# Kernel optimization log

Hardware: AMD Instinct MI355X
Metric: run time of the kernel (lower is better)

The kernel has to match this reference:

```python
import jax, jax.numpy as jnp
import numpy as np

TOP_K = 2


def setup_inputs() -> dict:
    key = jax.random.key(0)
    ks = jax.random.split(key, 5)
    B, S, H, F, E = 1, 2048, 1024, 3584, 8
    scale_h = 1.0 / np.sqrt(H)
    scale_f = 1.0 / np.sqrt(F)
    return {
        "hidden_states": jax.random.normal(ks[0], (B, S, H), dtype=jnp.float32),
        "gate_w": jax.random.normal(ks[1], (E, H), dtype=jnp.float32) * scale_h,
        "w1": jax.random.normal(ks[2], (E, H, F), dtype=jnp.float32) * scale_h,
        "w3": jax.random.normal(ks[3], (E, H, F), dtype=jnp.float32) * scale_h,
        "w2": jax.random.normal(ks[4], (E, F, H), dtype=jnp.float32) * scale_f,
    }


def reference(hidden_states, gate_w, w1, w2, w3):
    B, S, H = hidden_states.shape
    E = gate_w.shape[0]
    x = hidden_states.reshape(-1, H)  # [T, H]
    # Router: logits -> fp32 softmax -> top-k -> renormalize
    router_logits = x @ gate_w.T  # [T, E]
    probs = jax.nn.softmax(router_logits.astype(jnp.float32), axis=-1)
    top_w, top_idx = jax.lax.top_k(probs, TOP_K)  # [T, K]
    top_w = top_w / jnp.sum(top_w, axis=-1, keepdims=True)
    top_w = top_w.astype(x.dtype)
    # Dense combine weights [T, E]: routing weight if expert selected else 0
    combine = jnp.sum(jax.nn.one_hot(top_idx, E, dtype=x.dtype) * top_w[..., None], axis=1)
    # Per-expert SwiGLU FFN, weighted-summed (loop over small fixed E)
    out = jnp.zeros_like(x)
    for e in range(E):
        h = jax.nn.silu(x @ w1[e]) * (x @ w3[e])  # [T, F]
        out = out + (h @ w2[e]) * combine[:, e:e + 1]
    return out.reshape(B, S, H), router_logits
```

## Files before the change

kernel.cpp:

```cpp
#include <hip/hip_runtime.h>
#include <cstdint>
#include <cstddef>

#define Tt 2048
#define Hh 1024
#define Ff 3584
#define Ee 8
#define ROWS_CAP 5120

#define OFF_CTRL   0u
#define OFF_TOKE   256u
#define OFF_TOKW   (256u + 16384u)
#define OFF_ROWMAP (256u + 32768u)
#define OFF_ROWW   (256u + 32768u + 20480u)
#define OFF_XG     (1ull << 20)
#define OFF_G      (12ull << 20)

typedef __attribute__((ext_vector_type(8))) short bf16x8;
typedef __attribute__((ext_vector_type(4))) float f32x4;

__device__ __forceinline__ unsigned short f2bf(float f) {
  unsigned int u = __float_as_uint(f);
  u += 0x7fffu + ((u >> 16) & 1u);
  return (unsigned short)(u >> 16);
}

__device__ __forceinline__ unsigned pkbf(float a, float b) {
  unsigned r;
  asm("v_cvt_pk_bf16_f32 %0, %1, %2" : "=v"(r) : "v"(a), "v"(b));
  return r;
}

__device__ __forceinline__ void gload_lds16(const void* g, void* l) {
  auto gp = (const __attribute__((address_space(1))) char*)(uintptr_t)g;
  auto lp = (__attribute__((address_space(3))) char*)(uintptr_t)l;
  __builtin_amdgcn_global_load_lds(gp, lp, 16, 0, 0);
}

__device__ __forceinline__ bf16x8 frg(const char* lds, int row, int gc) {
  return *(const bf16x8*)(lds + row * 64 + ((gc ^ ((row >> 1) & 3)) * 16));
}

__global__ __launch_bounds__(256) void router_kernel(
    const float* __restrict__ x, const float* __restrict__ gw,
    float* __restrict__ logits_out, int* __restrict__ tok_e,
    float* __restrict__ tok_w, int* __restrict__ ctrl) {
  const int lane = threadIdx.x & 63;
  const int t = blockIdx.x * 4 + (threadIdx.x >> 6);
  const float4* xp = (const float4*)(x + (size_t)t * Hh + lane * 16);
  float4 x0 = xp[0], x1 = xp[1], x2 = xp[2], x3 = xp[3];
  float lg[Ee];
#pragma unroll
  for (int e = 0; e < Ee; ++e) {
    const float4* gp = (const float4*)(gw + e * Hh + lane * 16);
    float4 g0 = gp[0], g1 = gp[1], g2 = gp[2], g3 = gp[3];
    float s = x0.x*g0.x + x0.y*g0.y + x0.z*g0.z + x0.w*g0.w
            + x1.x*g1.x + x1.y*g1.y + x1.z*g1.z + x1.w*g1.w
            + x2.x*g2.x + x2.y*g2.y + x2.z*g2.z + x2.w*g2.w
            + x3.x*g3.x + x3.y*g3.y + x3.z*g3.z + x3.w*g3.w;
#pragma unroll
    for (int o = 32; o; o >>= 1) s += __shfl_xor(s, o);
    lg[e] = s;
  }
  if (lane == 0) {
    float m = lg[0];
#pragma unroll
    for (int e = 1; e < Ee; ++e) m = fmaxf(m, lg[e]);
    float p[Ee];
#pragma unroll
    for (int e = 0; e < Ee; ++e) p[e] = expf(lg[e] - m);
    int a0 = 0;
#pragma unroll
    for (int e = 1; e < Ee; ++e) if (p[e] > p[a0]) a0 = e;
    int a1 = (a0 == 0) ? 1 : 0;
#pragma unroll
    for (int e = 0; e < Ee; ++e) if (e != a0 && p[e] > p[a1]) a1 = e;
    float rs = p[a0] + p[a1];
    float w0 = p[a0] / rs, w1 = p[a1] / rs;
#pragma unroll
    for (int e = 0; e < Ee; ++e) logits_out[(size_t)t * Ee + e] = lg[e];
    tok_e[t * 2] = a0; tok_e[t * 2 + 1] = a1;
    tok_w[t * 2] = w0; tok_w[t * 2 + 1] = w1;
    atomicAdd(&ctrl[a0], 1); atomicAdd(&ctrl[a1], 1);
  }
}

__global__ void offsets_kernel(int* ctrl) {
  if (threadIdx.x == 0) {
    int acc = 0;
    for (int e = 0; e < Ee; ++e) {
      ctrl[16 + e] = acc;
      acc += ((ctrl[e] + 127) >> 7) << 7;
    }
    ctrl[16 + Ee] = acc;
  }
}

__global__ __launch_bounds__(512) void assign_kernel(
    int* ctrl, const int* __restrict__ tok_e, const float* __restrict__ tok_w,
    int* __restrict__ rowmap, float* __restrict__ roww) {
  int i = blockIdx.x * 512 + threadIdx.x;
  if (i < 2 * Tt) {
    int e = tok_e[i];
    int pos = atomicAdd(&ctrl[8 + e], 1);
    int r = ctrl[16 + e] + pos;
    rowmap[r] = i >> 1;
    roww[r] = tok_w[i];
  }
  if (i < Ee * 128) {
    int e = i >> 7, pd = i & 127;
    int o = ctrl[16 + e], o1 = ctrl[16 + e + 1], c = ctrl[e];
    int r = o + c + pd;
    if (r < o1) { rowmap[r] = -1; roww[r] = 0.f; }
  }
}

__global__ __launch_bounds__(128) void gather_kernel(
    const float* __restrict__ x, const int* __restrict__ ctrl,
    const int* __restrict__ rowmap, unsigned short* __restrict__ Xg) {
  int r = blockIdx.x;
  if (r >= ctrl[16 + Ee]) return;
  int t = rowmap[r];
  int j = threadIdx.x;
  uint4 v = make_uint4(0u, 0u, 0u, 0u);
  if (t >= 0) {
    const float4* xp = (const float4*)(x + (size_t)t * Hh + j * 8);
    float4 a = xp[0], b = xp[1];
    v.x = (unsigned)f2bf(a.x) | ((unsigned)f2bf(a.y) << 16);
    v.y = (unsigned)f2bf(a.z) | ((unsigned)f2bf(a.w) << 16);
    v.z = (unsigned)f2bf(b.x) | ((unsigned)f2bf(b.y) << 16);
    v.w = (unsigned)f2bf(b.z) | ((unsigned)f2bf(b.w) << 16);
  }
  *(uint4*)(Xg + (size_t)r * Hh + j * 8) = v;
}

__global__ __launch_bounds__(512, 4) void ffn13_fused(
    const unsigned short* __restrict__ Xg, const float* __restrict__ w1,
    const float* __restrict__ w3, const int* __restrict__ ctrl,
    unsigned short* __restrict__ G) {
  __shared__ alignas(16) char sA[2][8192], sB1[2][8192], sB3[2][8192];
  int lin = blockIdx.y * 28 + blockIdx.x;
  int xcd = lin & 7, idx = lin >> 3;
  int p = xcd + 8 * (idx >> 4);
  int mt = idx & 15;
  int e = p / 28, bx = p % 28;
  const int off0 = ctrl[16 + e], off1 = ctrl[16 + e + 1];
  const int row0 = off0 + mt * 128;
  if (row0 >= off1) return;
  const int n0 = bx * 128;
  const int tid = threadIdx.x, lane = tid & 63, wv = tid >> 6;
  const int wr = wv >> 2, wc = wv & 3;
  const float* w1e = w1 + (size_t)e * Hh * Ff;
  const float* w3e = w3 + (size_t)e * Hh * Ff;
  f32x4 acc1[4][2] = {};
  f32x4 acc3[4][2] = {};
  const int srow = wv * 16 + (lane >> 2);
  const int sgc = (lane & 3) ^ ((lane >> 3) & 3);
  const unsigned short* gA = Xg + (size_t)(row0 + srow) * Hh + sgc * 8;
  const int bn = tid & 127, bkq = tid >> 7;
  const int posB = bkq ^ ((bn >> 1) & 3);
  const int wofB = bn * 64 + posB * 16;
  const float* pB1 = w1e + (size_t)(bkq * 8) * Ff + n0 + bn;
  const float* pB3 = w3e + (size_t)(bkq * 8) * Ff + n0 + bn;
  float r1[8], r3[8];

  gload_lds16(gA, sA[0] + wv * 1024);
#pragma unroll
  for (int i = 0; i < 8; ++i) r1[i] = pB1[(size_t)i * Ff];
#pragma unroll
  for (int i = 0; i < 8; ++i) r3[i] = pB3[(size_t)i * Ff];
  {
    uint4 q;
    q.x = pkbf(r1[0], r1[1]); q.y = pkbf(r1[2], r1[3]);
    q.z = pkbf(r1[4], r1[5]); q.w = pkbf(r1[6], r1[7]);
    *(uint4*)(sB1[0] + wofB) = q;
    q.x = pkbf(r3[0], r3[1]); q.y = pkbf(r3[2], r3[3]);
    q.z = pkbf(r3[4], r3[5]); q.w = pkbf(r3[6], r3[7]);
    *(uint4*)(sB3[0] + wofB) = q;
  }
#pragma unroll
  for (int i = 0; i < 8; ++i) r1[i] = pB1[(size_t)(32 + i) * Ff];
#pragma unroll
  for (int i = 0; i < 8; ++i) r3[i] = pB3[(size_t)(32 + i) * Ff];
  asm volatile("s_waitcnt vmcnt(16) lgkmcnt(0)" ::: "memory");
  __builtin_amdgcn_s_barrier();
  __builtin_amdgcn_sched_barrier(0);

  for (int it = 0; it < 32; ++it) {
    const int cur = it & 1;
    if (it < 31) gload_lds16(gA + (size_t)(it + 1) * 32, sA[cur ^ 1] + wv * 1024);
    __builtin_amdgcn_sched_barrier(0);
    if (it < 31) {
      uint4 q;
      q.x = pkbf(r1[0], r1[1]); q.y = pkbf(r1[2], r1[3]);
      q.z = pkbf(r1[4], r1[5]); q.w = pkbf(r1[6], r1[7]);
      *(uint4*)(sB1[cur ^ 1] + wofB) = q;
      q.x = pkbf(r3[0], r3[1]); q.y = pkbf(r3[2], r3[3]);
      q.z = pkbf(r3[4], r3[5]); q.w = pkbf(r3[6], r3[7]);
      *(uint4*)(sB3[cur ^ 1] + wofB) = q;
    }
    if (it < 30) {
      const float* p1 = pB1 + (size_t)(it + 2) * 32 * Ff;
      const float* p3 = pB3 + (size_t)(it + 2) * 32 * Ff;
#pragma unroll
      for (int i = 0; i < 8; ++i) r1[i] = p1[(size_t)i * Ff];
#pragma unroll
      for (int i = 0; i < 8; ++i) r3[i] = p3[(size_t)i * Ff];
    }
    __builtin_amdgcn_sched_barrier(0);
    const int gc = lane >> 4;
    bf16x8 af[4];
#pragma unroll
    for (int mi = 0; mi < 4; ++mi)
      af[mi] = frg(sA[cur], wr * 64 + mi * 16 + (lane & 15), gc);
    __builtin_amdgcn_s_setprio(1);
#pragma unroll
    for (int ni = 0; ni < 2; ++ni) {
      bf16x8 b1 = frg(sB1[cur], wc * 32 + ni * 16 + (lane & 15), gc);
      bf16x8 b3 = frg(sB3[cur], wc * 32 + ni * 16 + (lane & 15), gc);
#pragma unroll
      for (int mi = 0; mi < 4; ++mi) {
        acc1[mi][ni] = __builtin_amdgcn_mfma_f32_16x16x32_bf16(af[mi], b1, acc1[mi][ni], 0, 0, 0);
        acc3[mi][ni] = __builtin_amdgcn_mfma_f32_16x16x32_bf16(af[mi], b3, acc3[mi][ni], 0, 0, 0);
      }
    }
    __builtin_amdgcn_s_setprio(0);
    if (it < 31) {
      if (it < 30) asm volatile("s_waitcnt vmcnt(16) lgkmcnt(0)" ::: "memory");
      else         asm volatile("s_waitcnt vmcnt(0) lgkmcnt(0)" ::: "memory");
      __builtin_amdgcn_s_barrier();
      __builtin_amdgcn_sched_barrier(0);
    }
  }
  const int rb = wr * 64 + 4 * (lane >> 4), cb = wc * 32 + (lane & 15);
#pragma unroll
  for (int mi = 0; mi < 4; ++mi)
#pragma unroll
    for (int ni = 0; ni < 2; ++ni)
#pragma unroll
      for (int r = 0; r < 4; ++r) {
        float h1 = acc1[mi][ni][r], h3 = acc3[mi][ni][r];
        float gv = h1 / (1.f + __expf(-h1)) * h3;
        G[(size_t)(row0 + rb + mi * 16 + r) * Ff + n0 + cb + ni * 16] = f2bf(gv);
      }
}

__global__ __launch_bounds__(512, 4) void ffn2_fused(
    const unsigned short* __restrict__ G, const float* __restrict__ w2,
    const int* __restrict__ ctrl, const int* __restrict__ rowmap,
    const float* __restrict__ roww, float* __restrict__ out) {
  __shared__ alignas(16) char sA[2][8192], sB[2][8192];
  int lin = (blockIdx.z * 128 + blockIdx.y) * 8 + blockIdx.x;
  int xcd = lin & 7, idx = lin >> 3;
  int e = idx >> 5, sub = idx & 31;
  int mt = sub >> 1, ks = sub & 1;
  int bx = xcd;
  const int off0 = ctrl[16 + e], off1 = ctrl[16 + e + 1];
  const int row0 = off0 + mt * 128;
  if (row0 >= off1) return;
  const int n0 = bx * 128;
  const int kb = ks * (Ff / 2);
  const int tid = threadIdx.x, lane = tid & 63, wv = tid >> 6;
  const int wr = wv >> 2, wc = wv & 3;
  const float* w2e = w2 + (size_t)e * Ff * Hh;
  f32x4 acc[4][2] = {};
  const int srow = wv * 16 + (lane >> 2);
  const int sgc = (lane & 3) ^ ((lane >> 3) & 3);
  const unsigned short* gA = G + (size_t)(row0 + srow) * Ff + kb + sgc * 8;
  const int bn = tid & 127, bkq = tid >> 7;
  const int posB = bkq ^ ((bn >> 1) & 3);
  const int wofB = bn * 64 + posB * 16;
  const float* pB = w2e + (size_t)(kb + bkq * 8) * Hh + n0 + bn;
  float r2[8];

  gload_lds16(gA, sA[0] + wv * 1024);
#pragma unroll
  for (int i = 0; i < 8; ++i) r2[i] = pB[(size_t)i * Hh];
  {
    uint4 q;
    q.x = pkbf(r2[0], r2[1]); q.y = pkbf(r2[2], r2[3]);
    q.z = pkbf(r2[4], r2[5]); q.w = pkbf(r2[6], r2[7]);
    *(uint4*)(sB[0] + wofB) = q;
  }
#pragma unroll
  for (int i = 0; i < 8; ++i) r2[i] = pB[(size_t)(32 + i) * Hh];
  asm volatile("s_waitcnt vmcnt(8) lgkmcnt(0)" ::: "memory");
  __builtin_amdgcn_s_barrier();
  __builtin_amdgcn_sched_barrier(0);

  const int NT = 56;
  for (int it = 0; it < NT; ++it) {
    const int cur = it & 1;
    if (it < NT - 1) gload_lds16(gA + (size_t)(it + 1) * 32, sA[cur ^ 1] + wv * 1024);
    __builtin_amdgcn_sched_barrier(0);
    if (it < NT - 1) {
      uint4 q;
      q.x = pkbf(r2[0], r2[1]); q.y = pkbf(r2[2], r2[3]);
      q.z = pkbf(r2[4], r2[5]); q.w = pkbf(r2[6], r2[7]);
      *(uint4*)(sB[cur ^ 1] + wofB) = q;
    }
    if (it < NT - 2) {
      const float* p2 = pB + (size_t)(it + 2) * 32 * Hh;
#pragma unroll
      for (int i = 0; i < 8; ++i) r2[i] = p2[(size_t)i * Hh];
    }
    __builtin_amdgcn_sched_barrier(0);
    const int gc = lane >> 4;
    bf16x8 af[4];
#pragma unroll
    for (int mi = 0; mi < 4; ++mi)
      af[mi] = frg(sA[cur], wr * 64 + mi * 16 + (lane & 15), gc);
    __builtin_amdgcn_s_setprio(1);
#pragma unroll
    for (int ni = 0; ni < 2; ++ni) {
      bf16x8 b = frg(sB[cur], wc * 32 + ni * 16 + (lane & 15), gc);
#pragma unroll
      for (int mi = 0; mi < 4; ++mi)
        acc[mi][ni] = __builtin_amdgcn_mfma_f32_16x16x32_bf16(af[mi], b, acc[mi][ni], 0, 0, 0);
    }
    __builtin_amdgcn_s_setprio(0);
    if (it < NT - 1) {
      if (it < NT - 2) asm volatile("s_waitcnt vmcnt(8) lgkmcnt(0)" ::: "memory");
      else             asm volatile("s_waitcnt vmcnt(0) lgkmcnt(0)" ::: "memory");
      __builtin_amdgcn_s_barrier();
      __builtin_amdgcn_sched_barrier(0);
    }
  }
  const int rb = wr * 64 + 4 * (lane >> 4), cb = wc * 32 + (lane & 15);
#pragma unroll
  for (int mi = 0; mi < 4; ++mi)
#pragma unroll
    for (int r = 0; r < 4; ++r) {
      int grow = row0 + rb + mi * 16 + r;
      int t = rowmap[grow];
      if (t < 0) continue;
      float wgt = roww[grow];
#pragma unroll
      for (int ni = 0; ni < 2; ++ni)
        atomicAdd(&out[(size_t)t * Hh + n0 + cb + ni * 16], wgt * acc[mi][ni][r]);
    }
}

extern "C" void kernel_launch(void* const* d_in, const int* in_sizes, int n_in,
                              void* d_out, int out_size, void* d_ws, size_t ws_size,
                              hipStream_t stream) {
  const float* x  = (const float*)d_in[0];
  const float* gw = (const float*)d_in[1];
  const float* w1 = (const float*)d_in[2];
  const float* w3 = (const float*)d_in[3];
  const float* w2 = (const float*)d_in[4];
  float* out = (float*)d_out;
  float* logits = out + (size_t)Tt * Hh;
  char* ws = (char*)d_ws;
  int* ctrl = (int*)(ws + OFF_CTRL);
  int* tok_e = (int*)(ws + OFF_TOKE);
  float* tok_w = (float*)(ws + OFF_TOKW);
  int* rowmap = (int*)(ws + OFF_ROWMAP);
  float* roww = (float*)(ws + OFF_ROWW);
  unsigned short* Xg = (unsigned short*)(ws + OFF_XG);
  unsigned short* G  = (unsigned short*)(ws + OFF_G);

  hipMemsetAsync(ctrl, 0, 256, stream);
  hipMemsetAsync(out, 0, (size_t)Tt * Hh * sizeof(float), stream);
  router_kernel<<<Tt / 4, 256, 0, stream>>>(x, gw, logits, tok_e, tok_w, ctrl);
  offsets_kernel<<<1, 64, 0, stream>>>(ctrl);
  assign_kernel<<<8, 512, 0, stream>>>(ctrl, tok_e, tok_w, rowmap, roww);
  gather_kernel<<<ROWS_CAP, 128, 0, stream>>>(x, ctrl, rowmap, Xg);
  ffn13_fused<<<dim3(28, 128), 512, 0, stream>>>(Xg, w1, w3, ctrl, G);
  ffn2_fused<<<dim3(8, 128, 2), 512, 0, stream>>>(G, w2, ctrl, rowmap, roww, out);
}
```

Before: 333.0 us.

## Deepen FFN GEMM pipelines to triple-buffered LDS with two-stage register prefetch

Both expert GEMM kernels move from double-buffered LDS with one stage of weight prefetch in registers to triple-buffered LDS with two alternating register sets. Global loads for weights are issued four K-steps ahead and the activation tile two steps ahead, so there is more time to hide memory latency on the strided fp32 weight reads. In exchange, LDS use per block rises by half and register pressure doubles for the prefetch buffers, which may lower occupancy at the 512x4 launch bounds. The workspace offsets for the routing arrays are also shifted.

Result: slower. 544.0 us (+63.4%).

```diff
diff --git a/kernel.cpp b/kernel.cpp
--- a/kernel.cpp
+++ b/kernel.cpp
@@ -9,10 +9,10 @@
 #define ROWS_CAP 5120
 
 #define OFF_CTRL   0u
-#define OFF_TOKE   256u
-#define OFF_TOKW   (256u + 16384u)
-#define OFF_ROWMAP (256u + 32768u)
-#define OFF_ROWW   (256u + 32768u + 20480u)
+#define OFF_TOKE   4096u
+#define OFF_TOKW   (4096u + 16384u)
+#define OFF_ROWMAP 65536u
+#define OFF_ROWW   98304u
 #define OFF_XG     (1ull << 20)
 #define OFF_G      (12ull << 20)
 
@@ -138,7 +138,7 @@
     const unsigned short* __restrict__ Xg, const float* __restrict__ w1,
     const float* __restrict__ w3, const int* __restrict__ ctrl,
     unsigned short* __restrict__ G) {
-  __shared__ alignas(16) char sA[2][8192], sB1[2][8192], sB3[2][8192];
+  __shared__ alignas(16) char bA[3][8192], bB1[3][8192], bB3[3][8192];
   int lin = blockIdx.y * 28 + blockIdx.x;
   int xcd = lin & 7, idx = lin >> 3;
   int p = xcd + 8 * (idx >> 4);
@@ -158,80 +158,101 @@
   const int sgc = (lane & 3) ^ ((lane >> 3) & 3);
   const unsigned short* gA = Xg + (size_t)(row0 + srow) * Hh + sgc * 8;
   const int bn = tid & 127, bkq = tid >> 7;
-  const int posB = bkq ^ ((bn >> 1) & 3);
-  const int wofB = bn * 64 + posB * 16;
+  const int wofB = bn * 64 + ((bkq ^ ((bn >> 1) & 3)) * 16);
   const float* pB1 = w1e + (size_t)(bkq * 8) * Ff + n0 + bn;
   const float* pB3 = w3e + (size_t)(bkq * 8) * Ff + n0 + bn;
-  float r1[8], r3[8];
-
-  gload_lds16(gA, sA[0] + wv * 1024);
-#pragma unroll
-  for (int i = 0; i < 8; ++i) r1[i] = pB1[(size_t)i * Ff];
-#pragma unroll
-  for (int i = 0; i < 8; ++i) r3[i] = pB3[(size_t)i * Ff];
+  float r1e[8], r3e[8], r1o[8], r3o[8];
+
+  char *cA = bA[0], *nA = bA[1], *xA = bA[2];
+  char *cB1 = bB1[0], *nB1 = bB1[1], *xB1 = bB1[2];
+  char *cB3 = bB3[0], *nB3 = bB3[1], *xB3 = bB3[2];
+
+#pragma unroll
+  for (int i = 0; i < 8; ++i) { r1e[i] = pB1[(size_t)i * Ff]; r3e[i] = pB3[(size_t)i * Ff]; }
+#pragma unroll
+  for (int i = 0; i < 8; ++i) { r1o[i] = pB1[(size_t)(32 + i) * Ff]; r3o[i] = pB3[(size_t)(32 + i) * Ff]; }
+  gload_lds16(gA, cA + wv * 1024);
+  __builtin_amdgcn_sched_barrier(0);
   {
     uint4 q;
-    q.x = pkbf(r1[0], r1[1]); q.y = pkbf(r1[2], r1[3]);
-    q.z = pkbf(r1[4], r1[5]); q.w = pkbf(r1[6], r1[7]);
-    *(uint4*)(sB1[0] + wofB) = q;
-    q.x = pkbf(r3[0], r3[1]); q.y = pkbf(r3[2], r3[3]);
-    q.z = pkbf(r3[4], r3[5]); q.w = pkbf(r3[6], r3[7]);
-    *(uint4*)(sB3[0] + wofB) = q;
-  }
-#pragma unroll
-  for (int i = 0; i < 8; ++i) r1[i] = pB1[(size_t)(32 + i) * Ff];
-#pragma unroll
-  for (int i = 0; i < 8; ++i) r3[i] = pB3[(size_t)(32 + i) * Ff];
-  asm volatile("s_waitcnt vmcnt(16) lgkmcnt(0)" ::: "memory");
+    q.x = pkbf(r1e[0], r1e[1]); q.y = pkbf(r1e[2], r1e[3]);
+    q.z = pkbf(r1e[4], r1e[5]); q.w = pkbf(r1e[6], r1e[7]);
+    *(uint4*)(cB1 + wofB) = q;
+    q.x = pkbf(r3e[0], r3e[1]); q.y = pkbf(r3e[2], r3e[3]);
+    q.z = pkbf(r3e[4], r3e[5]); q.w = pkbf(r3e[6], r3e[7]);
+    *(uint4*)(cB3 + wofB) = q;
+  }
+#pragma unroll
+  for (int i = 0; i < 8; ++i) { r1e[i] = pB1[(size_t)(64 + i) * Ff]; r3e[i] = pB3[(size_t)(64 + i) * Ff]; }
+  gload_lds16(gA + 32, nA + wv * 1024);
+  __builtin_amdgcn_sched_barrier(0);
+  {
+    uint4 q;
+    q.x = pkbf(r1o[0], r1o[1]); q.y = pkbf(r1o[2], r1o[3]);
+    q.z = pkbf(r1o[4], r1o[5]); q.w = pkbf(r1o[6], r1o[7]);
+    *(uint4*)(nB1 + wofB) = q;
+    q.x = pkbf(r3o[0], r3o[1]); q.y = pkbf(r3o[2], r3o[3]);
+    q.z = pkbf(r3o[4], r3o[5]); q.w = pkbf(r3o[6], r3o[7]);
+    *(uint4*)(nB3 + wofB) = q;
+  }
+#pragma unroll
+  for (int i = 0; i < 8; ++i) { r1o[i] = pB1[(size_t)(96 + i) * Ff]; r3o[i] = pB3[(size_t)(96 + i) * Ff]; }
+  asm volatile("s_waitcnt vmcnt(0) lgkmcnt(0)" ::: "memory");
   __builtin_amdgcn_s_barrier();
   __builtin_amdgcn_sched_barrier(0);
 
-  for (int it = 0; it < 32; ++it) {
-    const int cur = it & 1;
-    if (it < 31) gload_lds16(gA + (size_t)(it + 1) * 32, sA[cur ^ 1] + wv * 1024);
-    __builtin_amdgcn_sched_barrier(0);
-    if (it < 31) {
-      uint4 q;
-      q.x = pkbf(r1[0], r1[1]); q.y = pkbf(r1[2], r1[3]);
-      q.z = pkbf(r1[4], r1[5]); q.w = pkbf(r1[6], r1[7]);
-      *(uint4*)(sB1[cur ^ 1] + wofB) = q;
-      q.x = pkbf(r3[0], r3[1]); q.y = pkbf(r3[2], r3[3]);
-      q.z = pkbf(r3[4], r3[5]); q.w = pkbf(r3[6], r3[7]);
-      *(uint4*)(sB3[cur ^ 1] + wofB) = q;
-    }
-    if (it < 30) {
-      const float* p1 = pB1 + (size_t)(it + 2) * 32 * Ff;
-      const float* p3 = pB3 + (size_t)(it + 2) * 32 * Ff;
-#pragma unroll
-      for (int i = 0; i < 8; ++i) r1[i] = p1[(size_t)i * Ff];
-#pragma unroll
-      for (int i = 0; i < 8; ++i) r3[i] = p3[(size_t)i * Ff];
-    }
-    __builtin_amdgcn_sched_barrier(0);
-    const int gc = lane >> 4;
-    bf16x8 af[4];
-#pragma unroll
-    for (int mi = 0; mi < 4; ++mi)
-      af[mi] = frg(sA[cur], wr * 64 + mi * 16 + (lane & 15), gc);
-    __builtin_amdgcn_s_setprio(1);
-#pragma unroll
-    for (int ni = 0; ni < 2; ++ni) {
-      bf16x8 b1 = frg(sB1[cur], wc * 32 + ni * 16 + (lane & 15), gc);
-      bf16x8 b3 = frg(sB3[cur], wc * 32 + ni * 16 + (lane & 15), gc);
-#pragma unroll
-      for (int mi = 0; mi < 4; ++mi) {
-        acc1[mi][ni] = __builtin_amdgcn_mfma_f32_16x16x32_bf16(af[mi], b1, acc1[mi][ni], 0, 0, 0);
-        acc3[mi][ni] = __builtin_amdgcn_mfma_f32_16x16x32_bf16(af[mi], b3, acc3[mi][ni], 0, 0, 0);
-      }
-    }
-    __builtin_amdgcn_s_setprio(0);
-    if (it < 31) {
-      if (it < 30) asm volatile("s_waitcnt vmcnt(16) lgkmcnt(0)" ::: "memory");
-      else         asm volatile("s_waitcnt vmcnt(0) lgkmcnt(0)" ::: "memory");
-      __builtin_amdgcn_s_barrier();
-      __builtin_amdgcn_sched_barrier(0);
-    }
-  }
+#define H13_STEP(IT, R1, R3)                                                   \
+  {                                                                            \
+    if ((IT) < 30) gload_lds16(gA + (size_t)((IT) + 2) * 32, xA + wv * 1024);  \
+    __builtin_amdgcn_sched_barrier(0);                                         \
+    if ((IT) < 30) {                                                           \
+      uint4 q;                                                                 \
+      q.x = pkbf(R1[0], R1[1]); q.y = pkbf(R1[2], R1[3]);                      \
+      q.z = pkbf(R1[4], R1[5]); q.w = pkbf(R1[6], R1[7]);                      \
+      *(uint4*)(xB1 + wofB) = q;                                               \
+      q.x = pkbf(R3[0], R3[1]); q.y = pkbf(R3[2], R3[3]);                      \
+      q.z = pkbf(R3[4], R3[5]); q.w = pkbf(R3[6], R3[7]);                      \
+      *(uint4*)(xB3 + wofB) = q;                                               \
+    }                                                                          \
+    if ((IT) < 28) {                                                           \
+      const float* p1 = pB1 + (size_t)((IT) + 4) * 32 * Ff;                    \
+      const float* p3 = pB3 + (size_t)((IT) + 4) * 32 * Ff;                    \
+      _Pragma("unroll") for (int i = 0; i < 8; ++i) {                          \
+        R1[i] = p1[(size_t)i * Ff]; R3[i] = p3[(size_t)i * Ff]; }              \
+    }                                                                          \
+    __builtin_amdgcn_sched_barrier(0);                                         \
+    { const int gc = lane >> 4;                                                \
+      bf16x8 af[4];                                                            \
+      _Pragma("unroll") for (int mi = 0; mi < 4; ++mi)                         \
+        af[mi] = frg(cA, wr * 64 + mi * 16 + (lane & 15), gc);                 \
+      __builtin_amdgcn_s_setprio(1);                                           \
+      _Pragma("unroll") for (int ni = 0; ni < 2; ++ni) {                       \
+        bf16x8 b1 = frg(cB1, wc * 32 + ni * 16 + (lane & 15), gc);             \
+        bf16x8 b3 = frg(cB3, wc * 32 + ni * 16 + (lane & 15), gc);             \
+        _Pragma("unroll") for (int mi = 0; mi < 4; ++mi) {                     \
+          acc1[mi][ni] = __builtin_amdgcn_mfma_f32_16x16x32_bf16(af[mi], b1, acc1[mi][ni], 0, 0, 0); \
+          acc3[mi][ni] = __builtin_amdgcn_mfma_f32_16x16x32_bf16(af[mi], b3, acc3[mi][ni], 0, 0, 0); \
+        }                                                                      \
+      }                                                                        \
+      __builtin_amdgcn_s_setprio(0); }                                         \
+    if ((IT) < 31) {                                                           \
+      if ((IT) < 28)      asm volatile("s_waitcnt vmcnt(17) lgkmcnt(0)" ::: "memory"); \
+      else if ((IT) < 30) asm volatile("s_waitcnt vmcnt(1) lgkmcnt(0)" ::: "memory");  \
+      else                asm volatile("s_waitcnt vmcnt(0) lgkmcnt(0)" ::: "memory");  \
+      __builtin_amdgcn_s_barrier();                                            \
+      __builtin_amdgcn_sched_barrier(0);                                       \
+    }                                                                          \
+    { char* t_ = cA; cA = nA; nA = xA; xA = t_;                                \
+      t_ = cB1; cB1 = nB1; nB1 = xB1; xB1 = t_;                                \
+      t_ = cB3; cB3 = nB3; nB3 = xB3; xB3 = t_; }                              \
+  }
+
+  for (int j = 0; j < 16; ++j) {
+    H13_STEP(2 * j, r1e, r3e)
+    H13_STEP(2 * j + 1, r1o, r3o)
+  }
+#undef H13_STEP
+
   const int rb = wr * 64 + 4 * (lane >> 4), cb = wc * 32 + (lane & 15);
 #pragma unroll
   for (int mi = 0; mi < 4; ++mi)
@@ -249,7 +270,7 @@
     const unsigned short* __restrict__ G, const float* __restrict__ w2,
     const int* __restrict__ ctrl, const int* __restrict__ rowmap,
     const float* __restrict__ roww, float* __restrict__ out) {
-  __shared__ alignas(16) char sA[2][8192], sB[2][8192];
+  __shared__ alignas(16) char bA[3][8192], bB[3][8192];
   int lin = (blockIdx.z * 128 + blockIdx.y) * 8 + blockIdx.x;
   int xcd = lin & 7, idx = lin >> 3;
   int e = idx >> 5, sub = idx & 31;
@@ -268,64 +289,84 @@
   const int sgc = (lane & 3) ^ ((lane >> 3) & 3);
   const unsigned short* gA = G + (size_t)(row0 + srow) * Ff + kb + sgc * 8;
   const int bn = tid & 127, bkq = tid >> 7;
-  const int posB = bkq ^ ((bn >> 1) & 3);
-  const int wofB = bn * 64 + posB * 16;
+  const int wofB = bn * 64 + ((bkq ^ ((bn >> 1) & 3)) * 16);
   const float* pB = w2e + (size_t)(kb + bkq * 8) * Hh + n0 + bn;
-  float r2[8];
-
-  gload_lds16(gA, sA[0] + wv * 1024);
-#pragma unroll
-  for (int i = 0; i < 8; ++i) r2[i] = pB[(size_t)i * Hh];
+  float rbe[8], rbo[8];
+
+  char *cA = bA[0], *nA = bA[1], *xA = bA[2];
+  char *cB = bB[0], *nB = bB[1], *xB = bB[2];
+
+#pragma unroll
+  for (int i = 0; i < 8; ++i) rbe[i] = pB[(size_t)i * Hh];
+#pragma unroll
+  for (int i = 0; i < 8; ++i) rbo[i] = pB[(size_t)(32 + i) * Hh];
+  gload_lds16(gA, cA + wv * 1024);
+  __builtin_amdgcn_sched_barrier(0);
   {
     uint4 q;
-    q.x = pkbf(r2[0], r2[1]); q.y = pkbf(r2[2], r2[3]);
-    q.z = pkbf(r2[4], r2[5]); q.w = pkbf(r2[6], r2[7]);
-    *(uint4*)(sB[0] + wofB) = q;
-  }
-#pragma unroll
-  for (int i = 0; i < 8; ++i) r2[i] = pB[(size_t)(32 + i) * Hh];
-  asm volatile("s_waitcnt vmcnt(8) lgkmcnt(0)" ::: "memory");
+    q.x = pkbf(rbe[0], rbe[1]); q.y = pkbf(rbe[2], rbe[3]);
+    q.z = pkbf(rbe[4], rbe[5]); q.w = pkbf(rbe[6], rbe[7]);
+    *(uint4*)(cB + wofB) = q;
+  }
+#pragma unroll
+  for (int i = 0; i < 8; ++i) rbe[i] = pB[(size_t)(64 + i) * Hh];
+  gload_lds16(gA + 32, nA + wv * 1024);
+  __builtin_amdgcn_sched_barrier(0);
+  {
+    uint4 q;
+    q.x = pkbf(rbo[0], rbo[1]); q.y = pkbf(rbo[2], rbo[3]);
+    q.z = pkbf(rbo[4], rbo[5]); q.w = pkbf(rbo[6], rbo[7]);
+    *(uint4*)(nB + wofB) = q;
+  }
+#pragma unroll
+  for (int i = 0; i < 8; ++i) rbo[i] = pB[(size_t)(96 + i) * Hh];
+  asm volatile("s_waitcnt vmcnt(0) lgkmcnt(0)" ::: "memory");
   __builtin_amdgcn_s_barrier();
   __builtin_amdgcn_sched_barrier(0);
 
-  const int NT = 56;
-  for (int it = 0; it < NT; ++it) {
-    const int cur = it & 1;
-    if (it < NT - 1) gload_lds16(gA + (size_t)(it + 1) * 32, sA[cur ^ 1] + wv * 1024);
-    __builtin_amdgcn_sched_barrier(0);
-    if (it < NT - 1) {
-      uint4 q;
-      q.x = pkbf(r2[0], r2[1]); q.y = pkbf(r2[2], r2[3]);
-      q.z = pkbf(r2[4], r2[5]); q.w = pkbf(r2[6], r2[7]);
-      *(uint4*)(sB[cur ^ 1] + wofB) = q;
-    }
-    if (it < NT - 2) {
-      const float* p2 = pB + (size_t)(it + 2) * 32 * Hh;
-#pragma unroll
-      for (int i = 0; i < 8; ++i) r2[i] = p2[(size_t)i * Hh];
-    }
-    __builtin_amdgcn_sched_barrier(0);
-    const int gc = lane >> 4;
-    bf16x8 af[4];
-#pragma unroll
-    for (int mi = 0; mi < 4; ++mi)
-      af[mi] = frg(sA[cur], wr * 64 + mi * 16 + (lane & 15), gc);
-    __builtin_amdgcn_s_setprio(1);
-#pragma unroll
-    for (int ni = 0; ni < 2; ++ni) {
-      bf16x8 b = frg(sB[cur], wc * 32 + ni * 16 + (lane & 15), gc);
-#pragma unroll
-      for (int mi = 0; mi < 4; ++mi)
-        acc[mi][ni] = __builtin_amdgcn_mfma_f32_16x16x32_bf16(af[mi], b, acc[mi][ni], 0, 0, 0);
-    }
-    __builtin_amdgcn_s_setprio(0);
-    if (it < NT - 1) {
-      if (it < NT - 2) asm volatile("s_waitcnt vmcnt(8) lgkmcnt(0)" ::: "memory");
-      else             asm volatile("s_waitcnt vmcnt(0) lgkmcnt(0)" ::: "memory");
-      __builtin_amdgcn_s_barrier();
-      __builtin_amdgcn_sched_barrier(0);
-    }
-  }
+#define F2_STEP(IT, BS)                                                        \
+  {                                                                            \
+    if ((IT) < 54) gload_lds16(gA + (size_t)((IT) + 2) * 32, xA + wv * 1024);  \
+    __builtin_amdgcn_sched_barrier(0);                                         \
+    if ((IT) < 54) {                                                           \
+      uint4 q;                                                                 \
+      q.x = pkbf(BS[0], BS[1]); q.y = pkbf(BS[2], BS[3]);                      \
+      q.z = pkbf(BS[4], BS[5]); q.w = pkbf(BS[6], BS[7]);                      \
+      *(uint4*)(xB + wofB) = q;                                                \
+    }                                                                          \
+    if ((IT) < 52) {                                                           \
+      const float* pw = pB + (size_t)((IT) + 4) * 32 * Hh;                     \
+      _Pragma("unroll") for (int i = 0; i < 8; ++i) BS[i] = pw[(size_t)i * Hh];\
+    }                                                                          \
+    __builtin_amdgcn_sched_barrier(0);                                         \
+    { const int gc = lane >> 4;                                                \
+      bf16x8 af[4];                                                            \
+      _Pragma("unroll") for (int mi = 0; mi < 4; ++mi)                         \
+        af[mi] = frg(cA, wr * 64 + mi * 16 + (lane & 15), gc);                 \
+      __builtin_amdgcn_s_setprio(1);                                           \
+      _Pragma("unroll") for (int ni = 0; ni < 2; ++ni) {                       \
+        bf16x8 b = frg(cB, wc * 32 + ni * 16 + (lane & 15), gc);               \
+        _Pragma("unroll") for (int mi = 0; mi < 4; ++mi)                       \
+          acc[mi][ni] = __builtin_amdgcn_mfma_f32_16x16x32_bf16(af[mi], b, acc[mi][ni], 0, 0, 0); \
+      }                                                                        \
+      __builtin_amdgcn_s_setprio(0); }                                         \
+    if ((IT) < 55) {                                                           \
+      if ((IT) < 52)      asm volatile("s_waitcnt vmcnt(9) lgkmcnt(0)" ::: "memory"); \
+      else if ((IT) < 54) asm volatile("s_waitcnt vmcnt(1) lgkmcnt(0)" ::: "memory"); \
+      else                asm volatile("s_waitcnt vmcnt(0) lgkmcnt(0)" ::: "memory"); \
+      __builtin_amdgcn_s_barrier();                                            \
+      __builtin_amdgcn_sched_barrier(0);                                       \
+    }                                                                          \
+    { char* t_ = cA; cA = nA; nA = xA; xA = t_;                                \
+      t_ = cB; cB = nB; nB = xB; xB = t_; }                                    \
+  }
+
+  for (int j = 0; j < 28; ++j) {
+    F2_STEP(2 * j, rbe)
+    F2_STEP(2 * j + 1, rbo)
+  }
+#undef F2_STEP
+
   const int rb = wr * 64 + 4 * (lane >> 4), cb = wc * 32 + (lane & 15);
 #pragma unroll
   for (int mi = 0; mi < 4; ++mi)
```

## Build compact expert tile list to launch only populated tiles in FFN kernels

Applied to the files above, without the earlier changes.

The offsets kernel now writes a compact list of (expert, row0) pairs for each 128-row tile that actually holds tokens, capped at 40 tiles. Both FFN kernels index into this list instead of launching a grid for 16 tiles per expert and early-exiting the empty ones. This shrinks the grid from 3584/2048 workgroups to 1120/640 and changes the XCD-to-tile mapping. The prologue waitcnt is tightened to vmcnt(0), which may reduce early overlap, and the cap of 40 tiles assumes the padded row count never exceeds 5120 rows.

After: 349.3 us. 4.9% more time.

```diff
diff --git a/kernel.cpp b/kernel.cpp
--- a/kernel.cpp
+++ b/kernel.cpp
@@ -7,12 +7,13 @@
 #define Ff 3584
 #define Ee 8
 #define ROWS_CAP 5120
+#define MAXT 40
 
 #define OFF_CTRL   0u
-#define OFF_TOKE   256u
-#define OFF_TOKW   (256u + 16384u)
-#define OFF_ROWMAP (256u + 32768u)
-#define OFF_ROWW   (256u + 32768u + 20480u)
+#define OFF_TOKE   4096u
+#define OFF_TOKW   (4096u + 16384u)
+#define OFF_ROWMAP 65536u
+#define OFF_ROWW   98304u
 #define OFF_XG     (1ull << 20)
 #define OFF_G      (12ull << 20)
 
@@ -93,6 +94,16 @@
       acc += ((ctrl[e] + 127) >> 7) << 7;
     }
     ctrl[16 + Ee] = acc;
+    int idx = 0;
+    for (int e = 0; e < Ee; ++e) {
+      int nt = (ctrl[e] + 127) >> 7;
+      for (int m = 0; m < nt && idx < MAXT; ++m) {
+        ctrl[32 + 2 * idx] = e;
+        ctrl[33 + 2 * idx] = ctrl[16 + e] + m * 128;
+        ++idx;
+      }
+    }
+    for (; idx < MAXT; ++idx) { ctrl[32 + 2 * idx] = 0; ctrl[33 + 2 * idx] = -1; }
   }
 }
 
@@ -140,13 +151,11 @@
     unsigned short* __restrict__ G) {
   __shared__ alignas(16) char sA[2][8192], sB1[2][8192], sB3[2][8192];
   int lin = blockIdx.y * 28 + blockIdx.x;
-  int xcd = lin & 7, idx = lin >> 3;
-  int p = xcd + 8 * (idx >> 4);
-  int mt = idx & 15;
-  int e = p / 28, bx = p % 28;
-  const int off0 = ctrl[16 + e], off1 = ctrl[16 + e + 1];
-  const int row0 = off0 + mt * 128;
-  if (row0 >= off1) return;
+  int wg = (lin & 7) * 140 + (lin >> 3);
+  int bx = wg % 28, ft = wg / 28;
+  const int e = ctrl[32 + 2 * ft];
+  const int row0 = ctrl[33 + 2 * ft];
+  if (row0 < 0) return;
   const int n0 = bx * 128;
   const int tid = threadIdx.x, lane = tid & 63, wv = tid >> 6;
   const int wr = wv >> 2, wc = wv & 3;
@@ -158,13 +167,13 @@
   const int sgc = (lane & 3) ^ ((lane >> 3) & 3);
   const unsigned short* gA = Xg + (size_t)(row0 + srow) * Hh + sgc * 8;
   const int bn = tid & 127, bkq = tid >> 7;
-  const int posB = bkq ^ ((bn >> 1) & 3);
-  const int wofB = bn * 64 + posB * 16;
+  const int wofB = bn * 64 + ((bkq ^ ((bn >> 1) & 3)) * 16);
   const float* pB1 = w1e + (size_t)(bkq * 8) * Ff + n0 + bn;
   const float* pB3 = w3e + (size_t)(bkq * 8) * Ff + n0 + bn;
   float r1[8], r3[8];
 
   gload_lds16(gA, sA[0] + wv * 1024);
+  __builtin_amdgcn_sched_barrier(0);
 #pragma unroll
   for (int i = 0; i < 8; ++i) r1[i] = pB1[(size_t)i * Ff];
 #pragma unroll
@@ -182,7 +191,7 @@
   for (int i = 0; i < 8; ++i) r1[i] = pB1[(size_t)(32 + i) * Ff];
 #pragma unroll
   for (int i = 0; i < 8; ++i) r3[i] = pB3[(size_t)(32 + i) * Ff];
-  asm volatile("s_waitcnt vmcnt(16) lgkmcnt(0)" ::: "memory");
+  asm volatile("s_waitcnt vmcnt(0) lgkmcnt(0)" ::: "memory");
   __builtin_amdgcn_s_barrier();
   __builtin_amdgcn_sched_barrier(0);
 
@@ -208,23 +217,25 @@
       for (int i = 0; i < 8; ++i) r3[i] = p3[(size_t)i * Ff];
     }
     __builtin_amdgcn_sched_barrier(0);
-    const int gc = lane >> 4;
-    bf16x8 af[4];
-#pragma unroll
-    for (int mi = 0; mi < 4; ++mi)
-      af[mi] = frg(sA[cur], wr * 64 + mi * 16 + (lane & 15), gc);
-    __builtin_amdgcn_s_setprio(1);
-#pragma unroll
-    for (int ni = 0; ni < 2; ++ni) {
-      bf16x8 b1 = frg(sB1[cur], wc * 32 + ni * 16 + (lane & 15), gc);
-      bf16x8 b3 = frg(sB3[cur], wc * 32 + ni * 16 + (lane & 15), gc);
-#pragma unroll
-      for (int mi = 0; mi < 4; ++mi) {
-        acc1[mi][ni] = __builtin_amdgcn_mfma_f32_16x16x32_bf16(af[mi], b1, acc1[mi][ni], 0, 0, 0);
-        acc3[mi][ni] = __builtin_amdgcn_mfma_f32_16x16x32_bf16(af[mi], b3, acc3[mi][ni], 0, 0, 0);
+    {
+      const int gc = lane >> 4;
+      bf16x8 af[4];
+#pragma unroll
+      for (int mi = 0; mi < 4; ++mi)
+        af[mi] = frg(sA[cur], wr * 64 + mi * 16 + (lane & 15), gc);
+      __builtin_amdgcn_s_setprio(1);
+#pragma unroll
+      for (int ni = 0; ni < 2; ++ni) {
+        bf16x8 b1 = frg(sB1[cur], wc * 32 + ni * 16 + (lane & 15), gc);
+        bf16x8 b3 = frg(sB3[cur], wc * 32 + ni * 16 + (lane & 15), gc);
+#pragma unroll
+        for (int mi = 0; mi < 4; ++mi) {
+          acc1[mi][ni] = __builtin_amdgcn_mfma_f32_16x16x32_bf16(af[mi], b1, acc1[mi][ni], 0, 0, 0);
+          acc3[mi][ni] = __builtin_amdgcn_mfma_f32_16x16x32_bf16(af[mi], b3, acc3[mi][ni], 0, 0, 0);
+        }
       }
-    }
-    __builtin_amdgcn_s_setprio(0);
+      __builtin_amdgcn_s_setprio(0);
+    }
     if (it < 31) {
       if (it < 30) asm volatile("s_waitcnt vmcnt(16) lgkmcnt(0)" ::: "memory");
       else         asm volatile("s_waitcnt vmcnt(0) lgkmcnt(0)" ::: "memory");
@@ -250,14 +261,13 @@
     const int* __restrict__ ctrl, const int* __restrict__ rowmap,
     const float* __restrict__ roww, float* __restrict__ out) {
   __shared__ alignas(16) char sA[2][8192], sB[2][8192];
-  int lin = (blockIdx.z * 128 + blockIdx.y) * 8 + blockIdx.x;
-  int xcd = lin & 7, idx = lin >> 3;
-  int e = idx >> 5, sub = idx & 31;
-  int mt = sub >> 1, ks = sub & 1;
-  int bx = xcd;
-  const int off0 = ctrl[16 + e], off1 = ctrl[16 + e + 1];
-  const int row0 = off0 + mt * 128;
-  if (row0 >= off1) return;
+  int lin = (blockIdx.z * MAXT + blockIdx.y) * 8 + blockIdx.x;
+  int wg = (lin & 7) * 80 + (lin >> 3);
+  int bx = wg & 7, t2 = wg >> 3;
+  int ft = t2 % MAXT, ks = t2 / MAXT;
+  const int e = ctrl[32 + 2 * ft];
+  const int row0 = ctrl[33 + 2 * ft];
+  if (row0 < 0) return;
   const int n0 = bx * 128;
   const int kb = ks * (Ff / 2);
   const int tid = threadIdx.x, lane = tid & 63, wv = tid >> 6;
@@ -268,12 +278,12 @@
   const int sgc = (lane & 3) ^ ((lane >> 3) & 3);
   const unsigned short* gA = G + (size_t)(row0 + srow) * Ff + kb + sgc * 8;
   const int bn = tid & 127, bkq = tid >> 7;
-  const int posB = bkq ^ ((bn >> 1) & 3);
-  const int wofB = bn * 64 + posB * 16;
+  const int wofB = bn * 64 + ((bkq ^ ((bn >> 1) & 3)) * 16);
   const float* pB = w2e + (size_t)(kb + bkq * 8) * Hh + n0 + bn;
   float r2[8];
 
   gload_lds16(gA, sA[0] + wv * 1024);
+  __builtin_amdgcn_sched_barrier(0);
 #pragma unroll
   for (int i = 0; i < 8; ++i) r2[i] = pB[(size_t)i * Hh];
   {
@@ -284,7 +294,7 @@
   }
 #pragma unroll
   for (int i = 0; i < 8; ++i) r2[i] = pB[(size_t)(32 + i) * Hh];
-  asm volatile("s_waitcnt vmcnt(8) lgkmcnt(0)" ::: "memory");
+  asm volatile("s_waitcnt vmcnt(0) lgkmcnt(0)" ::: "memory");
   __builtin_amdgcn_s_barrier();
   __builtin_amdgcn_sched_barrier(0);
 
@@ -300,25 +310,27 @@
       *(uint4*)(sB[cur ^ 1] + wofB) = q;
     }
     if (it < NT - 2) {
-      const float* p2 = pB + (size_t)(it + 2) * 32 * Hh;
-#pragma unroll
-      for (int i = 0; i < 8; ++i) r2[i] = p2[(size_t)i * Hh];
+      const float* pw = pB + (size_t)(it + 2) * 32 * Hh;
+#pragma unroll
+      for (int i = 0; i < 8; ++i) r2[i] = pw[(size_t)i * Hh];
     }
     __builtin_amdgcn_sched_barrier(0);
-    const int gc = lane >> 4;
-    bf16x8 af[4];
-#pragma unroll
-    for (int mi = 0; mi < 4; ++mi)
-      af[mi] = frg(sA[cur], wr * 64 + mi * 16 + (lane & 15), gc);
-    __builtin_amdgcn_s_setprio(1);
-#pragma unroll
-    for (int ni = 0; ni < 2; ++ni) {
-      bf16x8 b = frg(sB[cur], wc * 32 + ni * 16 + (lane & 15), gc);
+    {
+      const int gc = lane >> 4;
+      bf16x8 af[4];
 #pragma unroll
       for (int mi = 0; mi < 4; ++mi)
-        acc[mi][ni] = __builtin_amdgcn_mfma_f32_16x16x32_bf16(af[mi], b, acc[mi][ni], 0, 0, 0);
-    }
-    __builtin_amdgcn_s_setprio(0);
+        af[mi] = frg(sA[cur], wr * 64 + mi * 16 + (lane & 15), gc);
+      __builtin_amdgcn_s_setprio(1);
+#pragma unroll
+      for (int ni = 0; ni < 2; ++ni) {
+        bf16x8 b = frg(sB[cur], wc * 32 + ni * 16 + (lane & 15), gc);
+#pragma unroll
+        for (int mi = 0; mi < 4; ++mi)
+          acc[mi][ni] = __builtin_amdgcn_mfma_f32_16x16x32_bf16(af[mi], b, acc[mi][ni], 0, 0, 0);
+      }
+      __builtin_amdgcn_s_setprio(0);
+    }
     if (it < NT - 1) {
       if (it < NT - 2) asm volatile("s_waitcnt vmcnt(8) lgkmcnt(0)" ::: "memory");
       else             asm volatile("s_waitcnt vmcnt(0) lgkmcnt(0)" ::: "memory");
@@ -360,12 +372,12 @@
   unsigned short* Xg = (unsigned short*)(ws + OFF_XG);
   unsigned short* G  = (unsigned short*)(ws + OFF_G);
 
-  hipMemsetAsync(ctrl, 0, 256, stream);
+  hipMemsetAsync(ctrl, 0, 512, stream);
   hipMemsetAsync(out, 0, (size_t)Tt * Hh * sizeof(float), stream);
   router_kernel<<<Tt / 4, 256, 0, stream>>>(x, gw, logits, tok_e, tok_w, ctrl);
   offsets_kernel<<<1, 64, 0, stream>>>(ctrl);
   assign_kernel<<<8, 512, 0, stream>>>(ctrl, tok_e, tok_w, rowmap, roww);
   gather_kernel<<<ROWS_CAP, 128, 0, stream>>>(x, ctrl, rowmap, Xg);
-  ffn13_fused<<<dim3(28, 128), 512, 0, stream>>>(Xg, w1, w3, ctrl, G);
-  ffn2_fused<<<dim3(8, 128, 2), 512, 0, stream>>>(G, w2, ctrl, rowmap, roww, out);
-}
+  ffn13_fused<<<dim3(28, MAXT), 512, 0, stream>>>(Xg, w1, w3, ctrl, G);
+  ffn2_fused<<<dim3(8, MAXT, 2), 512, 0, stream>>>(G, w2, ctrl, rowmap, roww, out);
+}
```
